# Optimization experiments

Hardware: AMD Instinct MI355X
Metric: run time of the kernel (lower is better)

## Reference

```python
import jax, jax.numpy as jnp
import numpy as np

B, L, K = 4096, 2048, 100
CLASSNUM = 2048
OFFSET = 1172  # ((L+K-1)*2-1 + K-1 - CLASSNUM) // 2 = (4392-2048)//2


def setup_inputs() -> dict:
    key = jax.random.key(0)
    ks = jax.random.split(key, 6)
    return {
        "x_real": jax.random.normal(ks[0], (B, L), jnp.float32),
        "x_imag": jax.random.normal(ks[1], (B, L), jnp.float32),
        "w1_real": jax.random.normal(ks[2], (K,), jnp.float32) * 0.1,
        "w1_imag": jax.random.normal(ks[3], (K,), jnp.float32) * 0.1,
        "wl_real": jax.random.normal(ks[4], (K,), jnp.float32) * 0.1,
        "wl_imag": jax.random.normal(ks[5], (K,), jnp.float32) * 0.1,
    }


def _conv_full_corr(x, w):
    # torch F.conv1d(x, w, padding=K-1): full cross-correlation.
    # jnp.convolve flips its 2nd arg (true convolution), so pre-flip w.
    return jax.vmap(lambda r: jnp.convolve(r, w[::-1], mode="full"))(x)


def _self_convolution(x):
    # convolution_std: F.conv1d(x, flip(x), padding=L-1) == true self-convolution
    # out[n] = sum_j x[j] * x[n-j]  (complex multiply, no conjugate)
    return jax.vmap(lambda r: jnp.convolve(r, r, mode="full"))(x)


def reference(x_real, x_imag, w1_real, w1_imag, wl_real, wl_imag):
    x = jax.lax.complex(x_real, x_imag)    # (B, 2048) complex64
    w1 = jax.lax.complex(w1_real, w1_imag)
    wl = jax.lax.complex(wl_real, wl_imag)
    x1 = _conv_full_corr(x, w1)            # (B, 2147)
    x1 = _self_convolution(x1)             # (B, 4293)
    x2 = _conv_full_corr(x1, wl)           # (B, 4392)
    return jnp.abs(x2[:, OFFSET:OFFSET + CLASSNUM])  # (B, 2048) float32
```

## Files before the change

kernel.cpp:

```cpp
#include <hip/hip_runtime.h>
#include <math.h>

#define NFFT  4096
#define LROW  2048
#define GLEN  298
#define HLEN  199
#define OFF   1172
#define NEG2PI_D (-6.283185307179586476925286766559)
#define NEG2PI_F (-6.28318530717958647692f)
#define RSQ2  0.70710678118654752440f

__device__ __forceinline__ int pad2(int i) { return i + (i >> 4); }

__device__ __forceinline__ float2 cadd(float2 a, float2 b) { return make_float2(a.x + b.x, a.y + b.y); }
__device__ __forceinline__ float2 csub(float2 a, float2 b) { return make_float2(a.x - b.x, a.y - b.y); }
__device__ __forceinline__ float2 cmul(float2 a, float2 b) {
  return make_float2(a.x * b.x - a.y * b.y, a.x * b.y + a.y * b.x);
}
__device__ __forceinline__ float2 cmni(float2 a) { return make_float2(a.y, -a.x); }

__device__ __forceinline__ void dft4(float2 a, float2 b, float2 c, float2 d,
                                     float2& F0, float2& F1, float2& F2, float2& F3) {
  const float2 s0 = cadd(a, c), s1 = csub(a, c);
  const float2 s2 = cadd(b, d), s3 = cmni(csub(b, d));
  F0 = cadd(s0, s2); F1 = cadd(s1, s3); F2 = csub(s0, s2); F3 = csub(s1, s3);
}

__device__ __forceinline__ void bf8(const float2 c[8], float2 e[8]) {
  float2 E0, E1, E2, E3, O0, O1, O2, O3;
  dft4(c[0], c[2], c[4], c[6], E0, E1, E2, E3);
  dft4(c[1], c[3], c[5], c[7], O0, O1, O2, O3);
  const float2 u0 = O0;
  const float2 u1 = make_float2(RSQ2 * (O1.x + O1.y), RSQ2 * (O1.y - O1.x));
  const float2 u2 = cmni(O2);
  const float2 u3 = make_float2(RSQ2 * (O3.y - O3.x), -RSQ2 * (O3.x + O3.y));
  e[0] = cadd(E0, u0); e[4] = csub(E0, u0);
  e[1] = cadd(E1, u1); e[5] = csub(E1, u1);
  e[2] = cadd(E2, u2); e[6] = csub(E2, u2);
  e[3] = cadd(E3, u3); e[7] = csub(E3, u3);
}

__global__ __launch_bounds__(256)
void prep_g_kernel(const float* __restrict__ w1r, const float* __restrict__ w1i,
                   const float* __restrict__ wlr, const float* __restrict__ wli,
                   float2* __restrict__ Ghat) {
  __shared__ float hr[HLEN], hs[HLEN], gr[GLEN], gi[GLEN];
  const int tid = threadIdx.x;
  for (int n = tid; n < HLEN; n += 256) {
    float sr = 0.f, si = 0.f;
    const int lo = n > 99 ? n - 99 : 0;
    const int hh = n < 99 ? n : 99;
    for (int i = lo; i <= hh; ++i) {
      const float ar = w1r[99 - i],       ai = w1i[99 - i];
      const float br = w1r[99 - (n - i)], bi = w1i[99 - (n - i)];
      sr += ar * br - ai * bi;
      si += ar * bi + ai * br;
    }
    hr[n] = sr; hs[n] = si;
  }
  __syncthreads();
  for (int n = tid; n < GLEN; n += 256) {
    float sr = 0.f, si = 0.f;
    const int lo = n > 99 ? n - 99 : 0;
    const int hh = n < 198 ? n : 198;
    for (int i = lo; i <= hh; ++i) {
      const float ar = hr[i],             ai = hs[i];
      const float br = wlr[99 - (n - i)], bi = wli[99 - (n - i)];
      sr += ar * br - ai * bi;
      si += ar * bi + ai * br;
    }
    gr[n] = sr; gi[n] = si;
  }
  __syncthreads();
  const int k = blockIdx.x * 256 + tid;
  double s, c;
  sincos(NEG2PI_D * (double)k / (double)NFFT, &s, &c);
  double cr = 1.0, ci = 0.0, accr = 0.0, acci = 0.0;
  for (int m = 0; m < GLEN; ++m) {
    const double a = (double)gr[m], b = (double)gi[m];
    accr += a * cr - b * ci;
    acci += a * ci + b * cr;
    const double t = cr * c - ci * s;
    ci = cr * s + ci * c;
    cr = t;
  }
  const double inv = 1.0 / (double)NFFT;
  const int p = ((k & 7) << 9) | (((k >> 3) & 7) << 6) | (((k >> 6) & 7) << 3) | (k >> 9);
  Ghat[p] = make_float2((float)(accr * inv), (float)(acci * inv));
}

template <int SH, bool PRE>
__device__ __forceinline__ void stage_ip(float2* A, const float2* __restrict__ Tw, int b) {
  const int M = 1 << SH;
  const int k = b & (M - 1);
  const int Q = b >> SH;
  const int base = (Q << (SH + 3)) + k;
  float2 c[8];
  #pragma unroll
  for (int t = 0; t < 8; ++t) c[t] = A[pad2(base + (t << SH))];
  const float2 w  = Tw[(NFFT >> (SH + 3)) * k];
  const float2 w2 = cmul(w, w),  w3 = cmul(w2, w),  w4 = cmul(w2, w2);
  const float2 w5 = cmul(w2, w3), w6 = cmul(w3, w3), w7 = cmul(w3, w4);
  float2 e[8];
  if (PRE) {
    c[1] = cmul(w,  c[1]); c[2] = cmul(w2, c[2]); c[3] = cmul(w3, c[3]);
    c[4] = cmul(w4, c[4]); c[5] = cmul(w5, c[5]); c[6] = cmul(w6, c[6]);
    c[7] = cmul(w7, c[7]);
    bf8(c, e);
  } else {
    bf8(c, e);
    e[1] = cmul(w,  e[1]); e[2] = cmul(w2, e[2]); e[3] = cmul(w3, e[3]);
    e[4] = cmul(w4, e[4]); e[5] = cmul(w5, e[5]); e[6] = cmul(w6, e[6]);
    e[7] = cmul(w7, e[7]);
  }
  #pragma unroll
  for (int t = 0; t < 8; ++t) A[pad2(base + (t << SH))] = e[t];
}

__global__ __launch_bounds__(512, 4)
void fft_conv_kernel(const float* __restrict__ xr, const float* __restrict__ xi,
                     const float2* __restrict__ Ghat, float* __restrict__ out) {
  __shared__ float2 A[4351];
  __shared__ float2 Tw[512];
  const int b = threadIdx.x;
  const int row = blockIdx.x;

  {
    float s, c;
    sincosf(NEG2PI_F * (float)b * (1.0f / (float)NFFT), &s, &c);
    Tw[b] = make_float2(c, s);
  }
  __syncthreads();

  {
    const float* xrr = xr + (size_t)row * LROW;
    const float* xir = xi + (size_t)row * LROW;
    float2 c[8];
    #pragma unroll
    for (int t = 0; t < 4; ++t) c[t] = make_float2(xrr[b + (t << 9)], xir[b + (t << 9)]);
    #pragma unroll
    for (int t = 4; t < 8; ++t) c[t] = make_float2(0.f, 0.f);
    float2 e[8];
    bf8(c, e);
    const float2 w  = Tw[b];
    const float2 w2 = cmul(w, w),  w3 = cmul(w2, w),  w4 = cmul(w2, w2);
    const float2 w5 = cmul(w2, w3), w6 = cmul(w3, w3), w7 = cmul(w3, w4);
    A[pad2(b)]              = e[0];
    A[pad2(b + (1 << 9))]   = cmul(w,  e[1]);
    A[pad2(b + (2 << 9))]   = cmul(w2, e[2]);
    A[pad2(b + (3 << 9))]   = cmul(w3, e[3]);
    A[pad2(b + (4 << 9))]   = cmul(w4, e[4]);
    A[pad2(b + (5 << 9))]   = cmul(w5, e[5]);
    A[pad2(b + (6 << 9))]   = cmul(w6, e[6]);
    A[pad2(b + (7 << 9))]   = cmul(w7, e[7]);
  }
  __syncthreads();
  stage_ip<6, false>(A, Tw, b);  __syncthreads();
  stage_ip<3, false>(A, Tw, b);  __syncthreads();

  {
    const int base = b << 3;
    float2 c[8];
    #pragma unroll
    for (int t = 0; t < 8; ++t) c[t] = A[pad2(base + t)];
    float2 e[8];
    bf8(c, e);
    const float4* G4 = reinterpret_cast<const float4*>(Ghat + base);
    float4 gq[4];
    #pragma unroll
    for (int q = 0; q < 4; ++q) gq[q] = G4[q];
    #pragma unroll
    for (int t = 0; t < 8; ++t) {
      const float2 x = e[t];
      const float2 x2 = make_float2(x.x * x.x - x.y * x.y, 2.f * x.x * x.y);
      const float2 g = (t & 1) ? make_float2(gq[t >> 1].z, gq[t >> 1].w)
                               : make_float2(gq[t >> 1].x, gq[t >> 1].y);
      const float2 z = cmul(x2, g);
      c[t] = make_float2(z.x, -z.y);
    }
    bf8(c, e);
    #pragma unroll
    for (int t = 0; t < 8; ++t) A[pad2(base + t)] = e[t];
  }
  __syncthreads();
  stage_ip<3, true>(A, Tw, b);   __syncthreads();
  stage_ip<6, true>(A, Tw, b);   __syncthreads();

  {
    float2 c[8];
    #pragma unroll
    for (int t = 0; t < 8; ++t) c[t] = A[pad2(b + (t << 9))];
    const float2 w  = Tw[b];
    const float2 w2 = cmul(w, w),  w3 = cmul(w2, w),  w4 = cmul(w2, w2);
    const float2 w5 = cmul(w2, w3), w6 = cmul(w3, w3), w7 = cmul(w3, w4);
    c[1] = cmul(w,  c[1]); c[2] = cmul(w2, c[2]); c[3] = cmul(w3, c[3]);
    c[4] = cmul(w4, c[4]); c[5] = cmul(w5, c[5]); c[6] = cmul(w6, c[6]);
    c[7] = cmul(w7, c[7]);
    float2 e[8];
    bf8(c, e);
    float* orow = out + (size_t)row * LROW;
    if (b >= 148) orow[b + 1024 - OFF] = sqrtf(e[2].x * e[2].x + e[2].y * e[2].y);
    orow[b + 1536 - OFF] = sqrtf(e[3].x * e[3].x + e[3].y * e[3].y);
    orow[b + 2048 - OFF] = sqrtf(e[4].x * e[4].x + e[4].y * e[4].y);
    orow[b + 2560 - OFF] = sqrtf(e[5].x * e[5].x + e[5].y * e[5].y);
    if (b < 148)  orow[b + 3072 - OFF] = sqrtf(e[6].x * e[6].x + e[6].y * e[6].y);
  }
}

extern "C" void kernel_launch(void* const* d_in, const int* in_sizes, int n_in,
                              void* d_out, int out_size, void* d_ws, size_t ws_size,
                              hipStream_t stream) {
  const float* xr  = (const float*)d_in[0];
  const float* xi  = (const float*)d_in[1];
  const float* w1r = (const float*)d_in[2];
  const float* w1i = (const float*)d_in[3];
  const float* wlr = (const float*)d_in[4];
  const float* wli = (const float*)d_in[5];
  float* out = (float*)d_out;
  float2* Ghat = (float2*)d_ws;
  const int rows = in_sizes[0] / LROW;

  prep_g_kernel<<<NFFT / 256, 256, 0, stream>>>(w1r, w1i, wlr, wli, Ghat);
  fft_conv_kernel<<<rows, 512, 0, stream>>>(xr, xi, Ghat, out);
}
```

Baseline: 187.8 us.

## Process two rows per block to share twiddles and halve barriers

Each block of the FFT convolution kernel now handles two rows in separate shared-memory buffers. The twiddle loads, twiddle-power computations, index math and __syncthreads barriers are shared across both rows, and the Ghat loads are reused. The twiddle table is also padded to avoid bank conflicts. This doubles LDS per block to about 74KB and raises register use, which can lower occupancy, and it assumes the row count is even.

```diff
diff --git a/kernel.cpp b/kernel.cpp
--- a/kernel.cpp
+++ b/kernel.cpp
@@ -90,120 +90,149 @@
 }
 
 template <int SH, bool PRE>
-__device__ __forceinline__ void stage_ip(float2* A, const float2* __restrict__ Tw, int b) {
+__device__ __forceinline__ void stage2(float2* __restrict__ A0, float2* __restrict__ A1,
+                                       const float2* __restrict__ Tw, int b) {
   const int M = 1 << SH;
   const int k = b & (M - 1);
   const int Q = b >> SH;
   const int base = (Q << (SH + 3)) + k;
-  float2 c[8];
+  int idx[8];
   #pragma unroll
-  for (int t = 0; t < 8; ++t) c[t] = A[pad2(base + (t << SH))];
-  const float2 w  = Tw[(NFFT >> (SH + 3)) * k];
+  for (int t = 0; t < 8; ++t) idx[t] = pad2(base + (t << SH));
+  const float2 w  = Tw[pad2((NFFT >> (SH + 3)) * k)];
   const float2 w2 = cmul(w, w),  w3 = cmul(w2, w),  w4 = cmul(w2, w2);
   const float2 w5 = cmul(w2, w3), w6 = cmul(w3, w3), w7 = cmul(w3, w4);
-  float2 e[8];
-  if (PRE) {
-    c[1] = cmul(w,  c[1]); c[2] = cmul(w2, c[2]); c[3] = cmul(w3, c[3]);
-    c[4] = cmul(w4, c[4]); c[5] = cmul(w5, c[5]); c[6] = cmul(w6, c[6]);
-    c[7] = cmul(w7, c[7]);
-    bf8(c, e);
-  } else {
-    bf8(c, e);
-    e[1] = cmul(w,  e[1]); e[2] = cmul(w2, e[2]); e[3] = cmul(w3, e[3]);
-    e[4] = cmul(w4, e[4]); e[5] = cmul(w5, e[5]); e[6] = cmul(w6, e[6]);
-    e[7] = cmul(w7, e[7]);
-  }
   #pragma unroll
-  for (int t = 0; t < 8; ++t) A[pad2(base + (t << SH))] = e[t];
+  for (int r = 0; r < 2; ++r) {
+    float2* A = r ? A1 : A0;
+    float2 c[8];
+    #pragma unroll
+    for (int t = 0; t < 8; ++t) c[t] = A[idx[t]];
+    float2 e[8];
+    if (PRE) {
+      c[1] = cmul(w,  c[1]); c[2] = cmul(w2, c[2]); c[3] = cmul(w3, c[3]);
+      c[4] = cmul(w4, c[4]); c[5] = cmul(w5, c[5]); c[6] = cmul(w6, c[6]);
+      c[7] = cmul(w7, c[7]);
+      bf8(c, e);
+    } else {
+      bf8(c, e);
+      e[1] = cmul(w,  e[1]); e[2] = cmul(w2, e[2]); e[3] = cmul(w3, e[3]);
+      e[4] = cmul(w4, e[4]); e[5] = cmul(w5, e[5]); e[6] = cmul(w6, e[6]);
+      e[7] = cmul(w7, e[7]);
+    }
+    #pragma unroll
+    for (int t = 0; t < 8; ++t) A[idx[t]] = e[t];
+  }
 }
 
 __global__ __launch_bounds__(512, 4)
 void fft_conv_kernel(const float* __restrict__ xr, const float* __restrict__ xi,
                      const float2* __restrict__ Ghat, float* __restrict__ out) {
-  __shared__ float2 A[4351];
-  __shared__ float2 Tw[512];
+  __shared__ float2 A0[4351], A1[4351];
+  __shared__ float2 Tw[543];
   const int b = threadIdx.x;
-  const int row = blockIdx.x;
+  const int row0 = blockIdx.x * 2;
 
   {
     float s, c;
     sincosf(NEG2PI_F * (float)b * (1.0f / (float)NFFT), &s, &c);
-    Tw[b] = make_float2(c, s);
-  }
-  __syncthreads();
-
-  {
-    const float* xrr = xr + (size_t)row * LROW;
-    const float* xir = xi + (size_t)row * LROW;
-    float2 c[8];
-    #pragma unroll
-    for (int t = 0; t < 4; ++t) c[t] = make_float2(xrr[b + (t << 9)], xir[b + (t << 9)]);
-    #pragma unroll
-    for (int t = 4; t < 8; ++t) c[t] = make_float2(0.f, 0.f);
-    float2 e[8];
-    bf8(c, e);
-    const float2 w  = Tw[b];
+    Tw[pad2(b)] = make_float2(c, s);
+  }
+  __syncthreads();
+
+  {
+    const float2 w  = Tw[pad2(b)];
     const float2 w2 = cmul(w, w),  w3 = cmul(w2, w),  w4 = cmul(w2, w2);
     const float2 w5 = cmul(w2, w3), w6 = cmul(w3, w3), w7 = cmul(w3, w4);
-    A[pad2(b)]              = e[0];
-    A[pad2(b + (1 << 9))]   = cmul(w,  e[1]);
-    A[pad2(b + (2 << 9))]   = cmul(w2, e[2]);
-    A[pad2(b + (3 << 9))]   = cmul(w3, e[3]);
-    A[pad2(b + (4 << 9))]   = cmul(w4, e[4]);
-    A[pad2(b + (5 << 9))]   = cmul(w5, e[5]);
-    A[pad2(b + (6 << 9))]   = cmul(w6, e[6]);
-    A[pad2(b + (7 << 9))]   = cmul(w7, e[7]);
-  }
-  __syncthreads();
-  stage_ip<6, false>(A, Tw, b);  __syncthreads();
-  stage_ip<3, false>(A, Tw, b);  __syncthreads();
+    int idx[8];
+    #pragma unroll
+    for (int t = 0; t < 8; ++t) idx[t] = pad2(b + (t << 9));
+    #pragma unroll
+    for (int r = 0; r < 2; ++r) {
+      float2* A = r ? A1 : A0;
+      const float* xrr = xr + (size_t)(row0 + r) * LROW;
+      const float* xir = xi + (size_t)(row0 + r) * LROW;
+      float2 c[8];
+      #pragma unroll
+      for (int t = 0; t < 4; ++t) c[t] = make_float2(xrr[b + (t << 9)], xir[b + (t << 9)]);
+      #pragma unroll
+      for (int t = 4; t < 8; ++t) c[t] = make_float2(0.f, 0.f);
+      float2 e[8];
+      bf8(c, e);
+      A[idx[0]] = e[0];
+      A[idx[1]] = cmul(w,  e[1]);
+      A[idx[2]] = cmul(w2, e[2]);
+      A[idx[3]] = cmul(w3, e[3]);
+      A[idx[4]] = cmul(w4, e[4]);
+      A[idx[5]] = cmul(w5, e[5]);
+      A[idx[6]] = cmul(w6, e[6]);
+      A[idx[7]] = cmul(w7, e[7]);
+    }
+  }
+  __syncthreads();
+  stage2<6, false>(A0, A1, Tw, b);  __syncthreads();
+  stage2<3, false>(A0, A1, Tw, b);  __syncthreads();
 
   {
     const int base = b << 3;
-    float2 c[8];
-    #pragma unroll
-    for (int t = 0; t < 8; ++t) c[t] = A[pad2(base + t)];
-    float2 e[8];
-    bf8(c, e);
+    int idx[8];
+    #pragma unroll
+    for (int t = 0; t < 8; ++t) idx[t] = pad2(base + t);
     const float4* G4 = reinterpret_cast<const float4*>(Ghat + base);
     float4 gq[4];
     #pragma unroll
     for (int q = 0; q < 4; ++q) gq[q] = G4[q];
     #pragma unroll
-    for (int t = 0; t < 8; ++t) {
-      const float2 x = e[t];
-      const float2 x2 = make_float2(x.x * x.x - x.y * x.y, 2.f * x.x * x.y);
-      const float2 g = (t & 1) ? make_float2(gq[t >> 1].z, gq[t >> 1].w)
-                               : make_float2(gq[t >> 1].x, gq[t >> 1].y);
-      const float2 z = cmul(x2, g);
-      c[t] = make_float2(z.x, -z.y);
-    }
-    bf8(c, e);
-    #pragma unroll
-    for (int t = 0; t < 8; ++t) A[pad2(base + t)] = e[t];
-  }
-  __syncthreads();
-  stage_ip<3, true>(A, Tw, b);   __syncthreads();
-  stage_ip<6, true>(A, Tw, b);   __syncthreads();
-
-  {
-    float2 c[8];
-    #pragma unroll
-    for (int t = 0; t < 8; ++t) c[t] = A[pad2(b + (t << 9))];
-    const float2 w  = Tw[b];
+    for (int r = 0; r < 2; ++r) {
+      float2* A = r ? A1 : A0;
+      float2 c[8];
+      #pragma unroll
+      for (int t = 0; t < 8; ++t) c[t] = A[idx[t]];
+      float2 e[8];
+      bf8(c, e);
+      #pragma unroll
+      for (int t = 0; t < 8; ++t) {
+        const float2 x = e[t];
+        const float2 x2 = make_float2(x.x * x.x - x.y * x.y, 2.f * x.x * x.y);
+        const float2 g = (t & 1) ? make_float2(gq[t >> 1].z, gq[t >> 1].w)
+                                 : make_float2(gq[t >> 1].x, gq[t >> 1].y);
+        const float2 z = cmul(x2, g);
+        c[t] = make_float2(z.x, -z.y);
+      }
+      bf8(c, e);
+      #pragma unroll
+      for (int t = 0; t < 8; ++t) A[idx[t]] = e[t];
+    }
+  }
+  __syncthreads();
+  stage2<3, true>(A0, A1, Tw, b);   __syncthreads();
+  stage2<6, true>(A0, A1, Tw, b);   __syncthreads();
+
+  {
+    const float2 w  = Tw[pad2(b)];
     const float2 w2 = cmul(w, w),  w3 = cmul(w2, w),  w4 = cmul(w2, w2);
     const float2 w5 = cmul(w2, w3), w6 = cmul(w3, w3), w7 = cmul(w3, w4);
-    c[1] = cmul(w,  c[1]); c[2] = cmul(w2, c[2]); c[3] = cmul(w3, c[3]);
-    c[4] = cmul(w4, c[4]); c[5] = cmul(w5, c[5]); c[6] = cmul(w6, c[6]);
-    c[7] = cmul(w7, c[7]);
-    float2 e[8];
-    bf8(c, e);
-    float* orow = out + (size_t)row * LROW;
-    if (b >= 148) orow[b + 1024 - OFF] = sqrtf(e[2].x * e[2].x + e[2].y * e[2].y);
-    orow[b + 1536 - OFF] = sqrtf(e[3].x * e[3].x + e[3].y * e[3].y);
-    orow[b + 2048 - OFF] = sqrtf(e[4].x * e[4].x + e[4].y * e[4].y);
-    orow[b + 2560 - OFF] = sqrtf(e[5].x * e[5].x + e[5].y * e[5].y);
-    if (b < 148)  orow[b + 3072 - OFF] = sqrtf(e[6].x * e[6].x + e[6].y * e[6].y);
+    int idx[8];
+    #pragma unroll
+    for (int t = 0; t < 8; ++t) idx[t] = pad2(b + (t << 9));
+    #pragma unroll
+    for (int r = 0; r < 2; ++r) {
+      float2* A = r ? A1 : A0;
+      float2 c[8];
+      #pragma unroll
+      for (int t = 0; t < 8; ++t) c[t] = A[idx[t]];
+      c[1] = cmul(w,  c[1]); c[2] = cmul(w2, c[2]); c[3] = cmul(w3, c[3]);
+      c[4] = cmul(w4, c[4]); c[5] = cmul(w5, c[5]); c[6] = cmul(w6, c[6]);
+      c[7] = cmul(w7, c[7]);
+      float2 e[8];
+      bf8(c, e);
+      float* orow = out + (size_t)(row0 + r) * LROW;
+      if (b >= 148) orow[b + 1024 - OFF] = sqrtf(e[2].x * e[2].x + e[2].y * e[2].y);
+      orow[b + 1536 - OFF] = sqrtf(e[3].x * e[3].x + e[3].y * e[3].y);
+      orow[b + 2048 - OFF] = sqrtf(e[4].x * e[4].x + e[4].y * e[4].y);
+      orow[b + 2560 - OFF] = sqrtf(e[5].x * e[5].x + e[5].y * e[5].y);
+      if (b < 148)  orow[b + 3072 - OFF] = sqrtf(e[6].x * e[6].x + e[6].y * e[6].y);
+    }
   }
 }
 
@@ -221,5 +250,5 @@
   const int rows = in_sizes[0] / LROW;
 
   prep_g_kernel<<<NFFT / 256, 256, 0, stream>>>(w1r, w1i, wlr, wli, Ghat);
-  fft_conv_kernel<<<rows, 512, 0, stream>>>(xr, xi, Ghat, out);
-}
+  fft_conv_kernel<<<rows / 2, 512, 0, stream>>>(xr, xi, Ghat, out);
+}
```

Result: no change. 186.9 us (-0.5%).

## Switch FFT from radix-8 four-pass to radix-16 three-pass with 256 threads

Applied to the files above, without the earlier changes.

Restructures the 4096-point forward and inverse FFTs from four radix-8 passes to three radix-16 passes, with 256 threads per row each handling 16 points. This cuts the number of shared-memory round trips and block barriers per row, and uses constant-multiply twiddles inside the radix-16 butterfly. The first stage also skips the zero-padded half of the input with a half-size butterfly. The trade-off is higher register pressure per thread and fewer threads per block, which may lower occupancy or latency hiding.

```diff
diff --git a/kernel.cpp b/kernel.cpp
--- a/kernel.cpp
+++ b/kernel.cpp
@@ -9,6 +9,8 @@
 #define NEG2PI_D (-6.283185307179586476925286766559)
 #define NEG2PI_F (-6.28318530717958647692f)
 #define RSQ2  0.70710678118654752440f
+#define C8    0.92387953251128675613f
+#define S8    0.38268343236508977173f
 
 __device__ __forceinline__ int pad2(int i) { return i + (i >> 4); }
 
@@ -18,6 +20,11 @@
   return make_float2(a.x * b.x - a.y * b.y, a.x * b.y + a.y * b.x);
 }
 __device__ __forceinline__ float2 cmni(float2 a) { return make_float2(a.y, -a.x); }
+__device__ __forceinline__ float2 tw1(float2 z){ return make_float2(C8*z.x + S8*z.y, C8*z.y - S8*z.x); }
+__device__ __forceinline__ float2 tw2(float2 z){ return make_float2(RSQ2*(z.x+z.y), RSQ2*(z.y-z.x)); }
+__device__ __forceinline__ float2 tw3(float2 z){ return make_float2(S8*z.x + C8*z.y, S8*z.y - C8*z.x); }
+__device__ __forceinline__ float2 tw6(float2 z){ return make_float2(RSQ2*(z.y-z.x), -RSQ2*(z.x+z.y)); }
+__device__ __forceinline__ float2 tw9(float2 z){ return make_float2(-(C8*z.x + S8*z.y), S8*z.x - C8*z.y); }
 
 __device__ __forceinline__ void dft4(float2 a, float2 b, float2 c, float2 d,
                                      float2& F0, float2& F1, float2& F2, float2& F3) {
@@ -26,18 +33,27 @@
   F0 = cadd(s0, s2); F1 = cadd(s1, s3); F2 = csub(s0, s2); F3 = csub(s1, s3);
 }
 
-__device__ __forceinline__ void bf8(const float2 c[8], float2 e[8]) {
-  float2 E0, E1, E2, E3, O0, O1, O2, O3;
-  dft4(c[0], c[2], c[4], c[6], E0, E1, E2, E3);
-  dft4(c[1], c[3], c[5], c[7], O0, O1, O2, O3);
-  const float2 u0 = O0;
-  const float2 u1 = make_float2(RSQ2 * (O1.x + O1.y), RSQ2 * (O1.y - O1.x));
-  const float2 u2 = cmni(O2);
-  const float2 u3 = make_float2(RSQ2 * (O3.y - O3.x), -RSQ2 * (O3.x + O3.y));
-  e[0] = cadd(E0, u0); e[4] = csub(E0, u0);
-  e[1] = cadd(E1, u1); e[5] = csub(E1, u1);
-  e[2] = cadd(E2, u2); e[6] = csub(E2, u2);
-  e[3] = cadd(E3, u3); e[7] = csub(E3, u3);
+__device__ __forceinline__ void dft16_tail(float2 Y0[4], float2 Y1[4], float2 Y2[4],
+                                           float2 Y3[4], float2 X[16]) {
+  Y1[1] = tw1(Y1[1]); Y1[2] = tw2(Y1[2]); Y1[3] = tw3(Y1[3]);
+  Y2[1] = tw2(Y2[1]); Y2[2] = cmni(Y2[2]); Y2[3] = tw6(Y2[3]);
+  Y3[1] = tw3(Y3[1]); Y3[2] = tw6(Y3[2]); Y3[3] = tw9(Y3[3]);
+  dft4(Y0[0], Y1[0], Y2[0], Y3[0], X[0], X[4], X[8],  X[12]);
+  dft4(Y0[1], Y1[1], Y2[1], Y3[1], X[1], X[5], X[9],  X[13]);
+  dft4(Y0[2], Y1[2], Y2[2], Y3[2], X[2], X[6], X[10], X[14]);
+  dft4(Y0[3], Y1[3], Y2[3], Y3[3], X[3], X[7], X[11], X[15]);
+}
+__device__ __forceinline__ void dft16(const float2 v[16], float2 X[16]) {
+  float2 Y0[4], Y1[4], Y2[4], Y3[4];
+  dft4(v[0], v[4], v[8],  v[12], Y0[0], Y0[1], Y0[2], Y0[3]);
+  dft4(v[1], v[5], v[9],  v[13], Y1[0], Y1[1], Y1[2], Y1[3]);
+  dft4(v[2], v[6], v[10], v[14], Y2[0], Y2[1], Y2[2], Y2[3]);
+  dft4(v[3], v[7], v[11], v[15], Y3[0], Y3[1], Y3[2], Y3[3]);
+  dft16_tail(Y0, Y1, Y2, Y3, X);
+}
+__device__ __forceinline__ void half4(float2 a, float2 d, float2 Y[4]) {
+  const float2 nd = cmni(d);
+  Y[0] = cadd(a, d); Y[1] = cadd(a, nd); Y[2] = csub(a, d); Y[3] = csub(a, nd);
 }
 
 __global__ __launch_bounds__(256)
@@ -85,125 +101,128 @@
     cr = t;
   }
   const double inv = 1.0 / (double)NFFT;
-  const int p = ((k & 7) << 9) | (((k >> 3) & 7) << 6) | (((k >> 6) & 7) << 3) | (k >> 9);
+  const int p = ((k & 15) << 8) | (k & 0xF0) | (k >> 8);
   Ghat[p] = make_float2((float)(accr * inv), (float)(acci * inv));
 }
 
-template <int SH, bool PRE>
-__device__ __forceinline__ void stage_ip(float2* A, const float2* __restrict__ Tw, int b) {
-  const int M = 1 << SH;
-  const int k = b & (M - 1);
-  const int Q = b >> SH;
-  const int base = (Q << (SH + 3)) + k;
-  float2 c[8];
+template <bool PRE>
+__device__ __forceinline__ void stageB(float2* A, const float2* __restrict__ Tw, int b) {
+  const int k = b & 15;
+  const int base = ((b >> 4) << 8) + k;
+  int idx[16];
   #pragma unroll
-  for (int t = 0; t < 8; ++t) c[t] = A[pad2(base + (t << SH))];
-  const float2 w  = Tw[(NFFT >> (SH + 3)) * k];
-  const float2 w2 = cmul(w, w),  w3 = cmul(w2, w),  w4 = cmul(w2, w2);
-  const float2 w5 = cmul(w2, w3), w6 = cmul(w3, w3), w7 = cmul(w3, w4);
-  float2 e[8];
+  for (int t = 0; t < 16; ++t) idx[t] = pad2(base + (t << 4));
+  float2 v[16];
+  #pragma unroll
+  for (int t = 0; t < 16; ++t) v[t] = A[idx[t]];
+  const float2 w = Tw[pad2(k << 4)];
   if (PRE) {
-    c[1] = cmul(w,  c[1]); c[2] = cmul(w2, c[2]); c[3] = cmul(w3, c[3]);
-    c[4] = cmul(w4, c[4]); c[5] = cmul(w5, c[5]); c[6] = cmul(w6, c[6]);
-    c[7] = cmul(w7, c[7]);
-    bf8(c, e);
-  } else {
-    bf8(c, e);
-    e[1] = cmul(w,  e[1]); e[2] = cmul(w2, e[2]); e[3] = cmul(w3, e[3]);
-    e[4] = cmul(w4, e[4]); e[5] = cmul(w5, e[5]); e[6] = cmul(w6, e[6]);
-    e[7] = cmul(w7, e[7]);
+    float2 wt = w;
+    v[1] = cmul(v[1], wt);
+    #pragma unroll
+    for (int t = 2; t < 16; ++t) { wt = cmul(wt, w); v[t] = cmul(v[t], wt); }
+  }
+  float2 X[16];
+  dft16(v, X);
+  if (!PRE) {
+    float2 wt = w;
+    X[1] = cmul(X[1], wt);
+    #pragma unroll
+    for (int t = 2; t < 16; ++t) { wt = cmul(wt, w); X[t] = cmul(X[t], wt); }
   }
   #pragma unroll
-  for (int t = 0; t < 8; ++t) A[pad2(base + (t << SH))] = e[t];
-}
-
-__global__ __launch_bounds__(512, 4)
+  for (int t = 0; t < 16; ++t) A[idx[t]] = X[t];
+}
+
+__global__ __launch_bounds__(256, 4)
 void fft_conv_kernel(const float* __restrict__ xr, const float* __restrict__ xi,
                      const float2* __restrict__ Ghat, float* __restrict__ out) {
   __shared__ float2 A[4351];
-  __shared__ float2 Tw[512];
+  __shared__ float2 Tw[271];
   const int b = threadIdx.x;
   const int row = blockIdx.x;
 
   {
     float s, c;
     sincosf(NEG2PI_F * (float)b * (1.0f / (float)NFFT), &s, &c);
-    Tw[b] = make_float2(c, s);
+    Tw[pad2(b)] = make_float2(c, s);
   }
   __syncthreads();
 
   {
     const float* xrr = xr + (size_t)row * LROW;
     const float* xir = xi + (size_t)row * LROW;
-    float2 c[8];
-    #pragma unroll
-    for (int t = 0; t < 4; ++t) c[t] = make_float2(xrr[b + (t << 9)], xir[b + (t << 9)]);
-    #pragma unroll
-    for (int t = 4; t < 8; ++t) c[t] = make_float2(0.f, 0.f);
-    float2 e[8];
-    bf8(c, e);
-    const float2 w  = Tw[b];
-    const float2 w2 = cmul(w, w),  w3 = cmul(w2, w),  w4 = cmul(w2, w2);
-    const float2 w5 = cmul(w2, w3), w6 = cmul(w3, w3), w7 = cmul(w3, w4);
-    A[pad2(b)]              = e[0];
-    A[pad2(b + (1 << 9))]   = cmul(w,  e[1]);
-    A[pad2(b + (2 << 9))]   = cmul(w2, e[2]);
-    A[pad2(b + (3 << 9))]   = cmul(w3, e[3]);
-    A[pad2(b + (4 << 9))]   = cmul(w4, e[4]);
-    A[pad2(b + (5 << 9))]   = cmul(w5, e[5]);
-    A[pad2(b + (6 << 9))]   = cmul(w6, e[6]);
-    A[pad2(b + (7 << 9))]   = cmul(w7, e[7]);
-  }
-  __syncthreads();
-  stage_ip<6, false>(A, Tw, b);  __syncthreads();
-  stage_ip<3, false>(A, Tw, b);  __syncthreads();
-
-  {
-    const int base = b << 3;
-    float2 c[8];
-    #pragma unroll
-    for (int t = 0; t < 8; ++t) c[t] = A[pad2(base + t)];
-    float2 e[8];
-    bf8(c, e);
+    float2 v[8];
+    #pragma unroll
+    for (int t = 0; t < 8; ++t)
+      v[t] = make_float2(xrr[b + (t << 8)], xir[b + (t << 8)]);
+    float2 Y0[4], Y1[4], Y2[4], Y3[4];
+    half4(v[0], v[4], Y0);
+    half4(v[1], v[5], Y1);
+    half4(v[2], v[6], Y2);
+    half4(v[3], v[7], Y3);
+    float2 X[16];
+    dft16_tail(Y0, Y1, Y2, Y3, X);
+    const float2 w = Tw[pad2(b)];
+    float2 wt = w;
+    X[1] = cmul(X[1], wt);
+    #pragma unroll
+    for (int t = 2; t < 16; ++t) { wt = cmul(wt, w); X[t] = cmul(X[t], wt); }
+    #pragma unroll
+    for (int t = 0; t < 16; ++t) A[pad2(b + (t << 8))] = X[t];
+  }
+  __syncthreads();
+  stageB<false>(A, Tw, b);  __syncthreads();
+
+  {
+    const int base = b << 4;
+    int idx[16];
+    #pragma unroll
+    for (int t = 0; t < 16; ++t) idx[t] = pad2(base + t);
+    float2 v[16];
+    #pragma unroll
+    for (int t = 0; t < 16; ++t) v[t] = A[idx[t]];
+    float2 X[16];
+    dft16(v, X);
     const float4* G4 = reinterpret_cast<const float4*>(Ghat + base);
-    float4 gq[4];
-    #pragma unroll
-    for (int q = 0; q < 4; ++q) gq[q] = G4[q];
-    #pragma unroll
-    for (int t = 0; t < 8; ++t) {
-      const float2 x = e[t];
+    float4 gq[8];
+    #pragma unroll
+    for (int q = 0; q < 8; ++q) gq[q] = G4[q];
+    #pragma unroll
+    for (int t = 0; t < 16; ++t) {
+      const float2 x = X[t];
       const float2 x2 = make_float2(x.x * x.x - x.y * x.y, 2.f * x.x * x.y);
       const float2 g = (t & 1) ? make_float2(gq[t >> 1].z, gq[t >> 1].w)
                                : make_float2(gq[t >> 1].x, gq[t >> 1].y);
       const float2 z = cmul(x2, g);
-      c[t] = make_float2(z.x, -z.y);
+      v[t] = make_float2(z.x, -z.y);
     }
-    bf8(c, e);
-    #pragma unroll
-    for (int t = 0; t < 8; ++t) A[pad2(base + t)] = e[t];
-  }
-  __syncthreads();
-  stage_ip<3, true>(A, Tw, b);   __syncthreads();
-  stage_ip<6, true>(A, Tw, b);   __syncthreads();
-
-  {
-    float2 c[8];
-    #pragma unroll
-    for (int t = 0; t < 8; ++t) c[t] = A[pad2(b + (t << 9))];
-    const float2 w  = Tw[b];
-    const float2 w2 = cmul(w, w),  w3 = cmul(w2, w),  w4 = cmul(w2, w2);
-    const float2 w5 = cmul(w2, w3), w6 = cmul(w3, w3), w7 = cmul(w3, w4);
-    c[1] = cmul(w,  c[1]); c[2] = cmul(w2, c[2]); c[3] = cmul(w3, c[3]);
-    c[4] = cmul(w4, c[4]); c[5] = cmul(w5, c[5]); c[6] = cmul(w6, c[6]);
-    c[7] = cmul(w7, c[7]);
-    float2 e[8];
-    bf8(c, e);
+    dft16(v, X);
+    #pragma unroll
+    for (int t = 0; t < 16; ++t) A[idx[t]] = X[t];
+  }
+  __syncthreads();
+  stageB<true>(A, Tw, b);   __syncthreads();
+
+  {
+    float2 v[16];
+    #pragma unroll
+    for (int t = 0; t < 16; ++t) v[t] = A[pad2(b + (t << 8))];
+    const float2 w = Tw[pad2(b)];
+    float2 wt = w;
+    v[1] = cmul(v[1], wt);
+    #pragma unroll
+    for (int t = 2; t < 16; ++t) { wt = cmul(wt, w); v[t] = cmul(v[t], wt); }
+    float2 X[16];
+    dft16(v, X);
     float* orow = out + (size_t)row * LROW;
-    if (b >= 148) orow[b + 1024 - OFF] = sqrtf(e[2].x * e[2].x + e[2].y * e[2].y);
-    orow[b + 1536 - OFF] = sqrtf(e[3].x * e[3].x + e[3].y * e[3].y);
-    orow[b + 2048 - OFF] = sqrtf(e[4].x * e[4].x + e[4].y * e[4].y);
-    orow[b + 2560 - OFF] = sqrtf(e[5].x * e[5].x + e[5].y * e[5].y);
-    if (b < 148)  orow[b + 3072 - OFF] = sqrtf(e[6].x * e[6].x + e[6].y * e[6].y);
+    if (b >= 148)
+      orow[b + 1024 - OFF] = sqrtf(X[4].x * X[4].x + X[4].y * X[4].y);
+    #pragma unroll
+    for (int j = 5; j < 12; ++j)
+      orow[b + (j << 8) - OFF] = sqrtf(X[j].x * X[j].x + X[j].y * X[j].y);
+    if (b < 148)
+      orow[b + 3072 - OFF] = sqrtf(X[12].x * X[12].x + X[12].y * X[12].y);
   }
 }
 
@@ -221,5 +240,5 @@
   const int rows = in_sizes[0] / LROW;
 
   prep_g_kernel<<<NFFT / 256, 256, 0, stream>>>(w1r, w1i, wlr, wli, Ghat);
-  fft_conv_kernel<<<rows, 512, 0, stream>>>(xr, xi, Ghat, out);
-}
+  fft_conv_kernel<<<rows, 256, 0, stream>>>(xr, xi, Ghat, out);
+}
```

Result: faster. 178.1 us (median of 2 runs) (-5.2%).
